# Kernel optimization log

Hardware: AMD Instinct MI355X
Metric: run time of the kernel (lower is better)

## Reference

```python
import jax, jax.numpy as jnp
from jax import lax
import numpy as np

LN_EPS = 1e-5


def _lstm_layer(x, w_ih, w_hh):
    """Single-layer LSTM, bias=False, batch_first. x: [B,T,I] -> hs: [B,T,H].
    PyTorch gate order: i, f, g, o along the 4H axis."""
    B, T, _ = x.shape
    H = w_hh.shape[1]
    # Precompute input projections for all timesteps in one GEMM: [B,T,4H]
    xg = jnp.einsum('bti,gi->btg', x, w_ih)

    def step(carry, xg_t):
        h, c = carry
        gates = xg_t + h @ w_hh.T  # [B,4H]
        i, f, g, o = jnp.split(gates, 4, axis=-1)
        c = jax.nn.sigmoid(f) * c + jax.nn.sigmoid(i) * jnp.tanh(g)
        h = jax.nn.sigmoid(o) * jnp.tanh(c)
        return (h, c), h

    init = (jnp.zeros((B, H), x.dtype), jnp.zeros((B, H), x.dtype))
    _, hs = lax.scan(step, init, jnp.swapaxes(xg, 0, 1))  # hs: [T,B,H]
    return jnp.swapaxes(hs, 0, 1)


def setup_inputs() -> dict:
    key = jax.random.key(0)
    ks = jax.random.split(key, 6)
    B, T, I, H, O = 256, 512, 1, 512, 1
    s_ih0 = 1.0 / np.sqrt(H)
    return {
        'input_seq': jax.random.normal(ks[0], (B, T, I), dtype=jnp.float32),
        'w_ih_l0': jax.random.normal(ks[1], (4 * H, I), dtype=jnp.float32) * s_ih0,
        'w_hh_l0': jax.random.normal(ks[2], (4 * H, H), dtype=jnp.float32) * s_ih0,
        'w_ih_l1': jax.random.normal(ks[3], (4 * H, H), dtype=jnp.float32) * s_ih0,
        'w_hh_l1': jax.random.normal(ks[4], (4 * H, H), dtype=jnp.float32) * s_ih0,
        'ln_gamma': jnp.ones((H,), dtype=jnp.float32),
        'ln_beta': jnp.zeros((H,), dtype=jnp.float32),
        'w_out': jax.random.normal(ks[5], (O, H), dtype=jnp.float32) * s_ih0,
    }


def reference(input_seq, w_ih_l0, w_hh_l0, w_ih_l1, w_hh_l1, ln_gamma, ln_beta, w_out):
    h1 = _lstm_layer(input_seq, w_ih_l0, w_hh_l0)  # [B,T,H]
    h2 = _lstm_layer(h1, w_ih_l1, w_hh_l1)         # [B,T,H]
    # Dropout is identity at inference. Only the last timestep is used downstream;
    # LayerNorm is per-position, so normalizing only h2[:, -1] matches the original.
    last = h2[:, -1, :]                             # [B,H]
    mu = jnp.mean(last, axis=-1, keepdims=True)
    var = jnp.mean(jnp.square(last - mu), axis=-1, keepdims=True)
    normed = (last - mu) * lax.rsqrt(var + LN_EPS) * ln_gamma + ln_beta
    return normed @ w_out.T                         # [B,1]
```

## Files before the change

kernel.cpp:

```cpp
#include <hip/hip_runtime.h>
#include <stdint.h>

#define BB 256
#define TT 512
#define HH 512
#define NBLK 256
#define SSTR 16
#define BBHH (BB*HH)

typedef __bf16 bf16x8 __attribute__((ext_vector_type(8)));
typedef float f32x4 __attribute__((ext_vector_type(4)));
typedef unsigned int u32x2 __attribute__((ext_vector_type(2)));

static __device__ __forceinline__ unsigned short f2bf(float f) {
    unsigned int u = __builtin_bit_cast(unsigned int, f);
    return (unsigned short)((u + 0x7fffu + ((u >> 16) & 1u)) >> 16);
}
static __device__ __forceinline__ bf16x8 packbf8(const float* p) {
    float4 a = *reinterpret_cast<const float4*>(p);
    float4 b = *reinterpret_cast<const float4*>(p + 4);
    unsigned short us[8] = { f2bf(a.x), f2bf(a.y), f2bf(a.z), f2bf(a.w),
                             f2bf(b.x), f2bf(b.y), f2bf(b.z), f2bf(b.w) };
    uint4 u; __builtin_memcpy(&u, us, 16);
    return __builtin_bit_cast(bf16x8, u);
}
static __device__ __forceinline__ float sigm(float x){ return 1.0f/(1.0f+__expf(-x)); }
static __device__ __forceinline__ float tanh_fast(float x){ return 2.0f/(1.0f+__expf(-2.0f*x)) - 1.0f; }

static __device__ __forceinline__ void ld_sys(uint4& d, const void* p) {
    asm volatile("global_load_dwordx4 %0, %1, off sc0 sc1" : "=v"(d) : "v"(p));
}
static __device__ __forceinline__ void st_sys2(void* p, u32x2 v) {
    asm volatile("global_store_dwordx2 %0, %1, off sc0 sc1" :: "v"(p), "v"(v) : "memory");
}
#define WAITVM(N) asm volatile("s_waitcnt vmcnt(" #N ")" ::: "memory")
#define SBAR      __builtin_amdgcn_sched_barrier(0)

__global__ __launch_bounds__(256) void prep_zero(unsigned short* __restrict__ h1p3,
                                                 unsigned short* __restrict__ h2p1,
                                                 int* __restrict__ slots) {
    int i = blockIdx.x * blockDim.x + threadIdx.x;
    for (int k = i; k < BBHH; k += gridDim.x * blockDim.x) { h1p3[k] = 0; h2p1[k] = 0; }
    if (i < NBLK * SSTR) slots[i] = 0;
}

__global__ __launch_bounds__(256, 1) void lstm_persist(
    const float* __restrict__ x,
    const float* __restrict__ wih0,
    const float* __restrict__ Whh0,
    const float* __restrict__ Wih1,
    const float* __restrict__ Whh1,
    unsigned short* __restrict__ h1buf,
    unsigned short* __restrict__ h2buf,
    int* __restrict__ slots)
{
    __shared__ float xf[16384];

    const int tid = threadIdx.x;
    const int w   = tid >> 6;
    const int l   = tid & 63;
    const int ln  = l & 15;
    const int kq  = l >> 4;
    const int bid = blockIdx.x;
    const bool isL0 = bid < 128;

    int g, cs, k0, mm = 0;
    const float* Wsrc;
    if (isL0) {
        g = bid >> 4; cs = bid & 15;
        k0 = w * 128;
        Wsrc = Whh0;
    } else {
        const int q = bid - 128;
        g = q >> 4; cs = q & 15;
        mm = w >> 1;
        k0 = (w & 1) * 256;
        Wsrc = mm ? Whh1 : Wih1;
    }

    bf16x8 wb[2][8][4];
    if (isL0) {
        #pragma unroll
        for (int nt = 0; nt < 2; ++nt)
            #pragma unroll
            for (int kb = 0; kb < 4; ++kb)
                #pragma unroll
                for (int g4 = 0; g4 < 4; ++g4)
                    wb[nt][kb][g4] = packbf8(Wsrc + (size_t)(g4 * HH + cs * 32 + nt * 16 + ln) * HH + k0 + kb * 32 + kq * 8);
    } else {
        #pragma unroll
        for (int nt = 0; nt < 2; ++nt)
            #pragma unroll
            for (int kb = 0; kb < 8; ++kb)
                #pragma unroll
                for (int g4 = 0; g4 < 4; ++g4)
                    wb[nt][kb][g4] = packbf8(Wsrc + (size_t)(g4 * HH + cs * 32 + nt * 16 + ln) * HH + k0 + kb * 32 + kq * 8);
    }

    const int erow = g * 32 + w * 8 + (l >> 3);
    f32x4 wiv[4] = {};
    if (isL0) {
        #pragma unroll
        for (int j = 0; j < 4; ++j) {
            const int cg = cs * 32 + (l & 7) * 4 + j;
            wiv[j] = (f32x4){ wih0[cg], wih0[512 + cg], wih0[1024 + cg], wih0[1536 + cg] };
        }
    }
    const int rt_r = w >> 1;
    const int rowl = (w & 1) * 8 + (l >> 3);
    const int nt_r = (l >> 2) & 1;
    const int colb = (l & 3) * 4;

    float cst[4] = {0.f, 0.f, 0.f, 0.f};

    for (int s = 0; s <= TT; ++s) {
        const bool active = isL0 ? (s < TT) : (s >= 1);
        if (active) {
            const int t = isL0 ? s : s - 1;
            const unsigned short* hp;
            if (isL0)    hp = h1buf + (size_t)((t - 1) & 3) * BBHH;
            else if (mm) hp = h2buf + (size_t)((t - 1) & 1) * BBHH;
            else         hp = h1buf + (size_t)(t & 3) * BBHH;

            float xv = 0.f;
            if (isL0) xv = x[(size_t)erow * TT + t];

            f32x4 acc[2][2][4];
            #pragma unroll
            for (int rt = 0; rt < 2; ++rt)
                #pragma unroll
                for (int nt = 0; nt < 2; ++nt)
                    #pragma unroll
                    for (int g4 = 0; g4 < 4; ++g4) acc[rt][nt][g4] = (f32x4){0.f,0.f,0.f,0.f};

            const char* ab = (const char*)(hp + (size_t)(g * 32 + ln) * HH + k0 + kq * 8);
            uint4 A[4][2];
            #pragma unroll
            for (int kb = 0; kb < 4; ++kb) {
                ld_sys(A[kb][0], ab + kb * 64);
                ld_sys(A[kb][1], ab + 16384 + kb * 64);
            }

            #define MK(kb, ap) do { \
                _Pragma("unroll") \
                for (int rt = 0; rt < 2; ++rt) { \
                    bf16x8 av = __builtin_bit_cast(bf16x8, A[ap][rt]); \
                    _Pragma("unroll") \
                    for (int nt = 0; nt < 2; ++nt) \
                        _Pragma("unroll") \
                        for (int g4 = 0; g4 < 4; ++g4) \
                            acc[rt][nt][g4] = __builtin_amdgcn_mfma_f32_16x16x32_bf16(av, wb[nt][kb][g4], acc[rt][nt][g4], 0, 0, 0); \
                } } while (0)

            if (isL0) {
                WAITVM(6); SBAR; MK(0, 0);
                WAITVM(4); SBAR; MK(1, 1);
                WAITVM(2); SBAR; MK(2, 2);
                WAITVM(0); SBAR; MK(3, 3);
            } else {
                WAITVM(6); SBAR; MK(0, 0);
                ld_sys(A[0][0], ab + 256); ld_sys(A[0][1], ab + 16384 + 256);
                WAITVM(6); SBAR; MK(1, 1);
                ld_sys(A[1][0], ab + 320); ld_sys(A[1][1], ab + 16384 + 320);
                WAITVM(6); SBAR; MK(2, 2);
                ld_sys(A[2][0], ab + 384); ld_sys(A[2][1], ab + 16384 + 384);
                WAITVM(6); SBAR; MK(3, 3);
                ld_sys(A[3][0], ab + 448); ld_sys(A[3][1], ab + 16384 + 448);
                WAITVM(6); SBAR; MK(4, 0);
                WAITVM(4); SBAR; MK(5, 1);
                WAITVM(2); SBAR; MK(6, 2);
                WAITVM(0); SBAR; MK(7, 3);
            }
            #undef MK

            #pragma unroll
            for (int rt = 0; rt < 2; ++rt)
                #pragma unroll
                for (int nt = 0; nt < 2; ++nt)
                    #pragma unroll
                    for (int r = 0; r < 4; ++r) {
                        const int row16 = kq * 4 + r;
                        f32x4 v = { acc[rt][nt][0][r], acc[rt][nt][1][r],
                                    acc[rt][nt][2][r], acc[rt][nt][3][r] };
                        *(f32x4*)((char*)xf + (((w * 2 + rt) * 2 + nt) * 16 + row16) * 256
                                            + ((ln * 16) ^ ((row16 & 7) << 4))) = v;
                    }
            __syncthreads();

            unsigned short* ho = isL0 ? (h1buf + (size_t)(t & 3) * BBHH)
                                      : (h2buf + (size_t)(t & 1) * BBHH);
            unsigned short hout[4];
            #pragma unroll
            for (int j = 0; j < 4; ++j) {
                f32x4 sv = (f32x4){0.f, 0.f, 0.f, 0.f};
                #pragma unroll
                for (int s4 = 0; s4 < 4; ++s4)
                    sv += *(const f32x4*)((const char*)xf + (((s4 * 2 + rt_r) * 2 + nt_r) * 16 + rowl) * 256
                                                          + (((colb + j) * 16) ^ ((rowl & 7) << 4)));
                if (isL0) sv += wiv[j] * xv;
                const float c = sigm(sv.y) * cst[j] + sigm(sv.x) * tanh_fast(sv.z);
                cst[j] = c;
                hout[j] = f2bf(sigm(sv.w) * tanh_fast(c));
            }
            u32x2 hv;
            hv.x = (unsigned int)hout[0] | ((unsigned int)hout[1] << 16);
            hv.y = (unsigned int)hout[2] | ((unsigned int)hout[3] << 16);
            st_sys2(ho + (size_t)erow * HH + cs * 32 + (l & 7) * 4, hv);
        }

        if (s < TT) {
            WAITVM(0);
            __syncthreads();
            if (active && tid == 0)
                __hip_atomic_store(slots + bid * SSTR, isL0 ? s + 1 : s,
                                   __ATOMIC_RELAXED, __HIP_MEMORY_SCOPE_AGENT);
            const int ns = s + 1;
            const bool nextAct = isL0 ? (ns < TT) : true;
            if (nextAct) {
                if (tid < 32) {
                    const int* sp;
                    int thr;
                    if (tid < 16) {
                        sp  = slots + (g * 16 + tid) * SSTR;
                        thr = ns;
                    } else {
                        sp  = slots + (128 + g * 16 + (tid - 16)) * SSTR;
                        thr = isL0 ? ns - 3 : ns - 1;
                    }
                    while (__hip_atomic_load(sp, __ATOMIC_RELAXED, __HIP_MEMORY_SCOPE_AGENT) < thr)
                        __builtin_amdgcn_s_sleep(2);
                }
                SBAR;
                __syncthreads();
            }
        }
    }
}

__global__ __launch_bounds__(64) void ln_out_k(const unsigned short* __restrict__ h2,
                                               const float* __restrict__ gamma,
                                               const float* __restrict__ beta,
                                               const float* __restrict__ wout,
                                               float* __restrict__ out)
{
    const int row = blockIdx.x;
    const int lane = threadIdx.x;
    uint4 u = *reinterpret_cast<const uint4*>(h2 + row * HH + lane * 8);
    unsigned short us[8];
    *reinterpret_cast<uint4*>(us) = u;
    float v[8];
    #pragma unroll
    for (int j = 0; j < 8; ++j) {
        unsigned int ww = ((unsigned int)us[j]) << 16;
        v[j] = __builtin_bit_cast(float, ww);
    }
    float sum = 0.f;
    #pragma unroll
    for (int j = 0; j < 8; ++j) sum += v[j];
    #pragma unroll
    for (int o = 32; o >= 1; o >>= 1) sum += __shfl_xor(sum, o);
    const float mu = sum * (1.0f / 512.0f);

    float vs = 0.f;
    #pragma unroll
    for (int j = 0; j < 8; ++j) { float d = v[j] - mu; vs += d * d; }
    #pragma unroll
    for (int o = 32; o >= 1; o >>= 1) vs += __shfl_xor(vs, o);
    const float inv = rsqrtf(vs * (1.0f / 512.0f) + 1e-5f);

    float dot = 0.f;
    #pragma unroll
    for (int j = 0; j < 8; ++j) {
        const int c = lane * 8 + j;
        dot += ((v[j] - mu) * inv * gamma[c] + beta[c]) * wout[c];
    }
    #pragma unroll
    for (int o = 32; o >= 1; o >>= 1) dot += __shfl_xor(dot, o);
    if (lane == 0) out[row] = dot;
}

extern "C" void kernel_launch(void* const* d_in, const int* in_sizes, int n_in,
                              void* d_out, int out_size, void* d_ws, size_t ws_size,
                              hipStream_t stream) {
    const float* x     = (const float*)d_in[0];
    const float* wih0  = (const float*)d_in[1];
    const float* whh0  = (const float*)d_in[2];
    const float* wih1  = (const float*)d_in[3];
    const float* whh1  = (const float*)d_in[4];
    const float* gamma = (const float*)d_in[5];
    const float* beta  = (const float*)d_in[6];
    const float* wout  = (const float*)d_in[7];

    char* ws = (char*)d_ws;
    unsigned short* h1buf = (unsigned short*)(ws);
    unsigned short* h2buf = (unsigned short*)(ws + (1024u << 10));
    int* slots            = (int*)(ws + (1536u << 10));

    hipLaunchKernelGGL(prep_zero, dim3(64), dim3(256), 0, stream,
                       h1buf + 3 * (size_t)BBHH, h2buf + BBHH, slots);

    hipLaunchKernelGGL(lstm_persist, dim3(NBLK), dim3(256), 0, stream,
                       x, wih0, whh0, wih1, whh1, h1buf, h2buf, slots);

    hipLaunchKernelGGL(ln_out_k, dim3(BB), dim3(64), 0, stream,
                       h2buf + BBHH, gamma, beta, wout, (float*)d_out);
}
```

Measured before the change: 2.738 ms.

## Double wavefronts per block and split K-reduction across eight waves

Raises the persistent LSTM kernel from 256 to 512 threads, so each wave handles half the K range and keeps half as many bf16 weight registers. Partial gate sums from the upper four waves are written to shared memory, the lower four waves add their own partials, and only those lower waves run the nonlinearity and store h. This aims to shorten the per-step serial MFMA chain and raise latency hiding inside the recurrent loop. In exchange it adds an extra shared-memory pass and one more block barrier per timestep, and the spin-wait sync code now runs with 512 threads.

```diff
diff --git a/kernel.cpp b/kernel.cpp
--- a/kernel.cpp
+++ b/kernel.cpp
@@ -44,7 +44,7 @@
     if (i < NBLK * SSTR) slots[i] = 0;
 }
 
-__global__ __launch_bounds__(256, 1) void lstm_persist(
+__global__ __launch_bounds__(512, 1) void lstm_persist(
     const float* __restrict__ x,
     const float* __restrict__ wih0,
     const float* __restrict__ Whh0,
@@ -68,45 +68,35 @@
     const float* Wsrc;
     if (isL0) {
         g = bid >> 4; cs = bid & 15;
-        k0 = w * 128;
+        k0 = w * 64;
         Wsrc = Whh0;
     } else {
         const int q = bid - 128;
         g = q >> 4; cs = q & 15;
-        mm = w >> 1;
-        k0 = (w & 1) * 256;
+        mm = w >> 2;
+        k0 = (w & 3) * 128;
         Wsrc = mm ? Whh1 : Wih1;
     }
-
-    bf16x8 wb[2][8][4];
-    if (isL0) {
-        #pragma unroll
-        for (int nt = 0; nt < 2; ++nt)
+    const int NKB = isL0 ? 2 : 4;
+
+    bf16x8 wb[2][4][4];
+    #pragma unroll
+    for (int nt = 0; nt < 2; ++nt)
+        for (int kb = 0; kb < NKB; ++kb)
             #pragma unroll
-            for (int kb = 0; kb < 4; ++kb)
-                #pragma unroll
-                for (int g4 = 0; g4 < 4; ++g4)
-                    wb[nt][kb][g4] = packbf8(Wsrc + (size_t)(g4 * HH + cs * 32 + nt * 16 + ln) * HH + k0 + kb * 32 + kq * 8);
-    } else {
-        #pragma unroll
-        for (int nt = 0; nt < 2; ++nt)
-            #pragma unroll
-            for (int kb = 0; kb < 8; ++kb)
-                #pragma unroll
-                for (int g4 = 0; g4 < 4; ++g4)
-                    wb[nt][kb][g4] = packbf8(Wsrc + (size_t)(g4 * HH + cs * 32 + nt * 16 + ln) * HH + k0 + kb * 32 + kq * 8);
-    }
-
-    const int erow = g * 32 + w * 8 + (l >> 3);
+            for (int g4 = 0; g4 < 4; ++g4)
+                wb[nt][kb][g4] = packbf8(Wsrc + (size_t)(g4 * HH + cs * 32 + nt * 16 + ln) * HH + k0 + kb * 32 + kq * 8);
+
+    const int erow = g * 32 + (w & 3) * 8 + (l >> 3);
     f32x4 wiv[4] = {};
-    if (isL0) {
+    if (isL0 && w < 4) {
         #pragma unroll
         for (int j = 0; j < 4; ++j) {
             const int cg = cs * 32 + (l & 7) * 4 + j;
             wiv[j] = (f32x4){ wih0[cg], wih0[512 + cg], wih0[1024 + cg], wih0[1536 + cg] };
         }
     }
-    const int rt_r = w >> 1;
+    const int rt_r = (w & 3) >> 1;
     const int rowl = (w & 1) * 8 + (l >> 3);
     const int nt_r = (l >> 2) & 1;
     const int colb = (l & 3) * 4;
@@ -122,9 +112,6 @@
             else if (mm) hp = h2buf + (size_t)((t - 1) & 1) * BBHH;
             else         hp = h1buf + (size_t)(t & 3) * BBHH;
 
-            float xv = 0.f;
-            if (isL0) xv = x[(size_t)erow * TT + t];
-
             f32x4 acc[2][2][4];
             #pragma unroll
             for (int rt = 0; rt < 2; ++rt)
@@ -135,11 +122,6 @@
 
             const char* ab = (const char*)(hp + (size_t)(g * 32 + ln) * HH + k0 + kq * 8);
             uint4 A[4][2];
-            #pragma unroll
-            for (int kb = 0; kb < 4; ++kb) {
-                ld_sys(A[kb][0], ab + kb * 64);
-                ld_sys(A[kb][1], ab + 16384 + kb * 64);
-            }
 
             #define MK(kb, ap) do { \
                 _Pragma("unroll") \
@@ -153,59 +135,83 @@
                 } } while (0)
 
             if (isL0) {
+                #pragma unroll
+                for (int kb = 0; kb < 2; ++kb) {
+                    ld_sys(A[kb][0], ab + kb * 64);
+                    ld_sys(A[kb][1], ab + 16384 + kb * 64);
+                }
+                WAITVM(2); SBAR; MK(0, 0);
+                WAITVM(0); SBAR; MK(1, 1);
+            } else {
+                #pragma unroll
+                for (int kb = 0; kb < 4; ++kb) {
+                    ld_sys(A[kb][0], ab + kb * 64);
+                    ld_sys(A[kb][1], ab + 16384 + kb * 64);
+                }
                 WAITVM(6); SBAR; MK(0, 0);
                 WAITVM(4); SBAR; MK(1, 1);
                 WAITVM(2); SBAR; MK(2, 2);
                 WAITVM(0); SBAR; MK(3, 3);
-            } else {
-                WAITVM(6); SBAR; MK(0, 0);
-                ld_sys(A[0][0], ab + 256); ld_sys(A[0][1], ab + 16384 + 256);
-                WAITVM(6); SBAR; MK(1, 1);
-                ld_sys(A[1][0], ab + 320); ld_sys(A[1][1], ab + 16384 + 320);
-                WAITVM(6); SBAR; MK(2, 2);
-                ld_sys(A[2][0], ab + 384); ld_sys(A[2][1], ab + 16384 + 384);
-                WAITVM(6); SBAR; MK(3, 3);
-                ld_sys(A[3][0], ab + 448); ld_sys(A[3][1], ab + 16384 + 448);
-                WAITVM(6); SBAR; MK(4, 0);
-                WAITVM(4); SBAR; MK(5, 1);
-                WAITVM(2); SBAR; MK(6, 2);
-                WAITVM(0); SBAR; MK(7, 3);
             }
             #undef MK
 
-            #pragma unroll
-            for (int rt = 0; rt < 2; ++rt)
-                #pragma unroll
-                for (int nt = 0; nt < 2; ++nt)
+            if (w >= 4) {
+                const int s4 = w - 4;
+                #pragma unroll
+                for (int rt = 0; rt < 2; ++rt)
                     #pragma unroll
-                    for (int r = 0; r < 4; ++r) {
-                        const int row16 = kq * 4 + r;
-                        f32x4 v = { acc[rt][nt][0][r], acc[rt][nt][1][r],
-                                    acc[rt][nt][2][r], acc[rt][nt][3][r] };
-                        *(f32x4*)((char*)xf + (((w * 2 + rt) * 2 + nt) * 16 + row16) * 256
-                                            + ((ln * 16) ^ ((row16 & 7) << 4))) = v;
-                    }
+                    for (int nt = 0; nt < 2; ++nt)
+                        #pragma unroll
+                        for (int r = 0; r < 4; ++r) {
+                            const int row16 = kq * 4 + r;
+                            f32x4 v = { acc[rt][nt][0][r], acc[rt][nt][1][r],
+                                        acc[rt][nt][2][r], acc[rt][nt][3][r] };
+                            *(f32x4*)((char*)xf + (((s4 * 2 + rt) * 2 + nt) * 16 + row16) * 256
+                                                + ((ln * 16) ^ ((row16 & 7) << 4))) = v;
+                        }
+            }
             __syncthreads();
-
-            unsigned short* ho = isL0 ? (h1buf + (size_t)(t & 3) * BBHH)
-                                      : (h2buf + (size_t)(t & 1) * BBHH);
-            unsigned short hout[4];
-            #pragma unroll
-            for (int j = 0; j < 4; ++j) {
-                f32x4 sv = (f32x4){0.f, 0.f, 0.f, 0.f};
-                #pragma unroll
-                for (int s4 = 0; s4 < 4; ++s4)
-                    sv += *(const f32x4*)((const char*)xf + (((s4 * 2 + rt_r) * 2 + nt_r) * 16 + rowl) * 256
-                                                          + (((colb + j) * 16) ^ ((rowl & 7) << 4)));
-                if (isL0) sv += wiv[j] * xv;
-                const float c = sigm(sv.y) * cst[j] + sigm(sv.x) * tanh_fast(sv.z);
-                cst[j] = c;
-                hout[j] = f2bf(sigm(sv.w) * tanh_fast(c));
-            }
-            u32x2 hv;
-            hv.x = (unsigned int)hout[0] | ((unsigned int)hout[1] << 16);
-            hv.y = (unsigned int)hout[2] | ((unsigned int)hout[3] << 16);
-            st_sys2(ho + (size_t)erow * HH + cs * 32 + (l & 7) * 4, hv);
+            if (w < 4) {
+                #pragma unroll
+                for (int rt = 0; rt < 2; ++rt)
+                    #pragma unroll
+                    for (int nt = 0; nt < 2; ++nt)
+                        #pragma unroll
+                        for (int r = 0; r < 4; ++r) {
+                            const int row16 = kq * 4 + r;
+                            char* p = (char*)xf + (((w * 2 + rt) * 2 + nt) * 16 + row16) * 256
+                                               + ((ln * 16) ^ ((row16 & 7) << 4));
+                            f32x4 v = *(const f32x4*)p;
+                            v.x += acc[rt][nt][0][r]; v.y += acc[rt][nt][1][r];
+                            v.z += acc[rt][nt][2][r]; v.w += acc[rt][nt][3][r];
+                            *(f32x4*)p = v;
+                        }
+            }
+            __syncthreads();
+
+            if (w < 4) {
+                float xv = 0.f;
+                if (isL0) xv = x[(size_t)erow * TT + t];
+                unsigned short* ho = isL0 ? (h1buf + (size_t)(t & 3) * BBHH)
+                                          : (h2buf + (size_t)(t & 1) * BBHH);
+                unsigned short hout[4];
+                #pragma unroll
+                for (int j = 0; j < 4; ++j) {
+                    f32x4 sv = (f32x4){0.f, 0.f, 0.f, 0.f};
+                    #pragma unroll
+                    for (int s4 = 0; s4 < 4; ++s4)
+                        sv += *(const f32x4*)((const char*)xf + (((s4 * 2 + rt_r) * 2 + nt_r) * 16 + rowl) * 256
+                                                              + (((colb + j) * 16) ^ ((rowl & 7) << 4)));
+                    if (isL0) sv += wiv[j] * xv;
+                    const float c = sigm(sv.y) * cst[j] + sigm(sv.x) * tanh_fast(sv.z);
+                    cst[j] = c;
+                    hout[j] = f2bf(sigm(sv.w) * tanh_fast(c));
+                }
+                u32x2 hv;
+                hv.x = (unsigned int)hout[0] | ((unsigned int)hout[1] << 16);
+                hv.y = (unsigned int)hout[2] | ((unsigned int)hout[3] << 16);
+                st_sys2(ho + (size_t)erow * HH + cs * 32 + (l & 7) * 4, hv);
+            }
         }
 
         if (s < TT) {
@@ -299,7 +305,7 @@
     hipLaunchKernelGGL(prep_zero, dim3(64), dim3(256), 0, stream,
                        h1buf + 3 * (size_t)BBHH, h2buf + BBHH, slots);
 
-    hipLaunchKernelGGL(lstm_persist, dim3(NBLK), dim3(256), 0, stream,
+    hipLaunchKernelGGL(lstm_persist, dim3(NBLK), dim3(512), 0, stream,
                        x, wih0, whh0, wih1, whh1, h1buf, h2buf, slots);
 
     hipLaunchKernelGGL(ln_out_k, dim3(BB), dim3(64), 0, stream,
```

Result: slower. 6.549 ms (+139.2%).

## Replace block-level barrier sync with per-wave flags and issue all h loads upfront

Applied to the files above, without the earlier changes.

Each wave now publishes its own progress flag and polls the flags of the producer waves itself, so the per-step __syncthreads around the cross-block handshake is removed. Layer-1 blocks issue all eight h-tile loads at once instead of a rolling window of four. The x load moves after the MFMA phase, and a barrier is added before the LDS write. The intent is to shorten the critical path of each recurrent step, at the cost of more flag traffic (4x slots, 64 lanes polling per wave) and more registers for the load buffers. Because prep_zero now clears slots unconditionally, it depends on the launch grid size matching the larger slot array.

```diff
diff --git a/kernel.cpp b/kernel.cpp
--- a/kernel.cpp
+++ b/kernel.cpp
@@ -41,7 +41,7 @@
                                                  int* __restrict__ slots) {
     int i = blockIdx.x * blockDim.x + threadIdx.x;
     for (int k = i; k < BBHH; k += gridDim.x * blockDim.x) { h1p3[k] = 0; h2p1[k] = 0; }
-    if (i < NBLK * SSTR) slots[i] = 0;
+    slots[i] = 0;
 }
 
 __global__ __launch_bounds__(256, 1) void lstm_persist(
@@ -77,25 +77,15 @@
         k0 = (w & 1) * 256;
         Wsrc = mm ? Whh1 : Wih1;
     }
+    const int NKB = isL0 ? 4 : 8;
 
     bf16x8 wb[2][8][4];
-    if (isL0) {
-        #pragma unroll
-        for (int nt = 0; nt < 2; ++nt)
-            #pragma unroll
-            for (int kb = 0; kb < 4; ++kb)
-                #pragma unroll
-                for (int g4 = 0; g4 < 4; ++g4)
-                    wb[nt][kb][g4] = packbf8(Wsrc + (size_t)(g4 * HH + cs * 32 + nt * 16 + ln) * HH + k0 + kb * 32 + kq * 8);
-    } else {
-        #pragma unroll
-        for (int nt = 0; nt < 2; ++nt)
-            #pragma unroll
-            for (int kb = 0; kb < 8; ++kb)
-                #pragma unroll
-                for (int g4 = 0; g4 < 4; ++g4)
-                    wb[nt][kb][g4] = packbf8(Wsrc + (size_t)(g4 * HH + cs * 32 + nt * 16 + ln) * HH + k0 + kb * 32 + kq * 8);
-    }
+    #pragma unroll
+    for (int nt = 0; nt < 2; ++nt)
+        for (int kb = 0; kb < NKB; ++kb)
+            #pragma unroll
+            for (int g4 = 0; g4 < 4; ++g4)
+                wb[nt][kb][g4] = packbf8(Wsrc + (size_t)(g4 * HH + cs * 32 + nt * 16 + ln) * HH + k0 + kb * 32 + kq * 8);
 
     const int erow = g * 32 + w * 8 + (l >> 3);
     f32x4 wiv[4] = {};
@@ -111,6 +101,11 @@
     const int nt_r = (l >> 2) & 1;
     const int colb = (l & 3) * 4;
 
+    const int bb = l >> 2, ww = l & 3;
+    const int sidL0 = ((g * 16 + bb) * 4 + ww) * SSTR;
+    const int sidL1 = ((128 + g * 16 + bb) * 4 + ww) * SSTR;
+    int* const myslot = slots + (bid * 4 + w) * SSTR;
+
     float cst[4] = {0.f, 0.f, 0.f, 0.f};
 
     for (int s = 0; s <= TT; ++s) {
@@ -122,9 +117,6 @@
             else if (mm) hp = h2buf + (size_t)((t - 1) & 1) * BBHH;
             else         hp = h1buf + (size_t)(t & 3) * BBHH;
 
-            float xv = 0.f;
-            if (isL0) xv = x[(size_t)erow * TT + t];
-
             f32x4 acc[2][2][4];
             #pragma unroll
             for (int rt = 0; rt < 2; ++rt)
@@ -134,17 +126,12 @@
                     for (int g4 = 0; g4 < 4; ++g4) acc[rt][nt][g4] = (f32x4){0.f,0.f,0.f,0.f};
 
             const char* ab = (const char*)(hp + (size_t)(g * 32 + ln) * HH + k0 + kq * 8);
-            uint4 A[4][2];
-            #pragma unroll
-            for (int kb = 0; kb < 4; ++kb) {
-                ld_sys(A[kb][0], ab + kb * 64);
-                ld_sys(A[kb][1], ab + 16384 + kb * 64);
-            }
-
-            #define MK(kb, ap) do { \
+            uint4 A[8][2];
+
+            #define MK(kb) do { \
                 _Pragma("unroll") \
                 for (int rt = 0; rt < 2; ++rt) { \
-                    bf16x8 av = __builtin_bit_cast(bf16x8, A[ap][rt]); \
+                    bf16x8 av = __builtin_bit_cast(bf16x8, A[kb][rt]); \
                     _Pragma("unroll") \
                     for (int nt = 0; nt < 2; ++nt) \
                         _Pragma("unroll") \
@@ -153,26 +140,33 @@
                 } } while (0)
 
             if (isL0) {
-                WAITVM(6); SBAR; MK(0, 0);
-                WAITVM(4); SBAR; MK(1, 1);
-                WAITVM(2); SBAR; MK(2, 2);
-                WAITVM(0); SBAR; MK(3, 3);
+                #pragma unroll
+                for (int kb = 0; kb < 4; ++kb) {
+                    ld_sys(A[kb][0], ab + kb * 64);
+                    ld_sys(A[kb][1], ab + 16384 + kb * 64);
+                }
+                WAITVM(6); SBAR; MK(0);
+                WAITVM(4); SBAR; MK(1);
+                WAITVM(2); SBAR; MK(2);
+                WAITVM(0); SBAR; MK(3);
             } else {
-                WAITVM(6); SBAR; MK(0, 0);
-                ld_sys(A[0][0], ab + 256); ld_sys(A[0][1], ab + 16384 + 256);
-                WAITVM(6); SBAR; MK(1, 1);
-                ld_sys(A[1][0], ab + 320); ld_sys(A[1][1], ab + 16384 + 320);
-                WAITVM(6); SBAR; MK(2, 2);
-                ld_sys(A[2][0], ab + 384); ld_sys(A[2][1], ab + 16384 + 384);
-                WAITVM(6); SBAR; MK(3, 3);
-                ld_sys(A[3][0], ab + 448); ld_sys(A[3][1], ab + 16384 + 448);
-                WAITVM(6); SBAR; MK(4, 0);
-                WAITVM(4); SBAR; MK(5, 1);
-                WAITVM(2); SBAR; MK(6, 2);
-                WAITVM(0); SBAR; MK(7, 3);
+                #pragma unroll
+                for (int kb = 0; kb < 8; ++kb) {
+                    ld_sys(A[kb][0], ab + kb * 64);
+                    ld_sys(A[kb][1], ab + 16384 + kb * 64);
+                }
+                WAITVM(14); SBAR; MK(0);
+                WAITVM(12); SBAR; MK(1);
+                WAITVM(10); SBAR; MK(2);
+                WAITVM(8);  SBAR; MK(3);
+                WAITVM(6);  SBAR; MK(4);
+                WAITVM(4);  SBAR; MK(5);
+                WAITVM(2);  SBAR; MK(6);
+                WAITVM(0);  SBAR; MK(7);
             }
             #undef MK
 
+            __syncthreads();
             #pragma unroll
             for (int rt = 0; rt < 2; ++rt)
                 #pragma unroll
@@ -187,6 +181,8 @@
                     }
             __syncthreads();
 
+            float xv = 0.f;
+            if (isL0) xv = x[(size_t)erow * TT + t];
             unsigned short* ho = isL0 ? (h1buf + (size_t)(t & 3) * BBHH)
                                       : (h2buf + (size_t)(t & 1) * BBHH);
             unsigned short hout[4];
@@ -210,28 +206,24 @@
 
         if (s < TT) {
             WAITVM(0);
-            __syncthreads();
-            if (active && tid == 0)
-                __hip_atomic_store(slots + bid * SSTR, isL0 ? s + 1 : s,
+            if (active && l == 0)
+                __hip_atomic_store(myslot, isL0 ? s + 1 : s,
                                    __ATOMIC_RELAXED, __HIP_MEMORY_SCOPE_AGENT);
             const int ns = s + 1;
             const bool nextAct = isL0 ? (ns < TT) : true;
             if (nextAct) {
-                if (tid < 32) {
-                    const int* sp;
-                    int thr;
-                    if (tid < 16) {
-                        sp  = slots + (g * 16 + tid) * SSTR;
-                        thr = ns;
-                    } else {
-                        sp  = slots + (128 + g * 16 + (tid - 16)) * SSTR;
-                        thr = isL0 ? ns - 3 : ns - 1;
-                    }
-                    while (__hip_atomic_load(sp, __ATOMIC_RELAXED, __HIP_MEMORY_SCOPE_AGENT) < thr)
-                        __builtin_amdgcn_s_sleep(2);
+                const int thrOwn = isL0 ? ns : ns - 1;
+                const int thrOth = isL0 ? ns - 3 : ns;
+                const int* pOwn = slots + (isL0 ? sidL0 : sidL1);
+                const int* pOth = slots + (isL0 ? sidL1 : sidL0);
+                bool okA = false, okB = false;
+                while (true) {
+                    if (!okA) okA = __hip_atomic_load(pOwn, __ATOMIC_RELAXED, __HIP_MEMORY_SCOPE_AGENT) >= thrOwn;
+                    if (!okB) okB = __hip_atomic_load(pOth, __ATOMIC_RELAXED, __HIP_MEMORY_SCOPE_AGENT) >= thrOth;
+                    if (okA && okB) break;
+                    __builtin_amdgcn_s_sleep(1);
                 }
                 SBAR;
-                __syncthreads();
             }
         }
     }
```

Result: slower. 6.912 ms (+152.5%).
